# Kernel optimization log

Measured on AMD Instinct MI355X. Metric: run time of the kernel, lower is better.

The kernel has to match this reference:

```python
import jax, jax.numpy as jnp
import numpy as np
from jax import lax

NUM_CLASSES = 5
CONF_THRESH = 0.6
NMS_THRESH = 0.2
NUM_TOPK = 64          # min(topk=1000, 64) as in post_process
STRIDES = (8, 16, 32)
FMP = ((160, 160), (80, 80), (40, 40))  # 1280x1280 input
BATCH = 128


def setup_inputs() -> dict:
    key = jax.random.key(0)
    ks = jax.random.split(key, 9)
    d = {}
    i = 0
    for name, (h, w) in zip(("8", "16", "32"), FMP):
        hw = h * w
        d["obj" + name] = jax.random.normal(ks[i], (BATCH, hw, 1), jnp.float32); i += 1
        d["cls" + name] = jax.random.normal(ks[i], (BATCH, hw, NUM_CLASSES), jnp.float32); i += 1
        d["reg" + name] = jax.random.normal(ks[i], (BATCH, hw, 4), jnp.float32); i += 1
    return d


def make_anchors(h, w, stride):
    ay, ax = jnp.meshgrid(jnp.arange(h), jnp.arange(w), indexing="ij")
    xy = jnp.stack([ax, ay], axis=-1).astype(jnp.float32).reshape(-1, 2)
    return (xy + 0.5) * stride  # [HW, 2]


def decode_boxes(reg, anchors, stride):
    # ctr = reg[:, :2]*stride + anchor;  wh = exp(reg[:, 2:])*stride
    ctr = reg[:, :2] * stride + anchors
    wh = jnp.exp(reg[:, 2:]) * stride
    return jnp.concatenate([ctr - 0.5 * wh, ctr + 0.5 * wh], axis=-1)  # x1y1x2y2


def iou_matrix(b):
    # Faithful to YOLO.nms: areas un-clamped, intersection w/h clamped at 1e-10
    x1, y1, x2, y2 = b[:, 0], b[:, 1], b[:, 2], b[:, 3]
    areas = (x2 - x1) * (y2 - y1)
    xx1 = jnp.maximum(x1[:, None], x1[None, :])
    yy1 = jnp.maximum(y1[:, None], y1[None, :])
    xx2 = jnp.minimum(x2[:, None], x2[None, :])
    yy2 = jnp.minimum(y2[:, None], y2[None, :])
    w = jnp.maximum(1e-10, xx2 - xx1)
    h = jnp.maximum(1e-10, yy2 - yy1)
    inter = w * h
    return inter / (areas[:, None] + areas[None, :] - inter)


def nms_keep(iou, valid):
    # Greedy NMS on score-sorted candidates: fixed-length sequential suppression.
    n = iou.shape[0]
    idx = jnp.arange(n)
    def body(i, keep):
        sup = keep[i] & (iou[i] > NMS_THRESH) & (idx > i)
        return keep & jnp.logical_not(sup)
    return lax.fori_loop(0, n, body, valid)


def _single_image(obj8, cls8, reg8, obj16, cls16, reg16, obj32, cls32, reg32):
    levels = ((obj8, cls8, reg8), (obj16, cls16, reg16), (obj32, cls32, reg32))
    sc, lb, bx, vd = [], [], [], []
    for lvl, (obj, cls, reg) in enumerate(levels):
        h, w = FMP[lvl]
        s = STRIDES[lvl]
        anchors = make_anchors(h, w, s)
        boxes = decode_boxes(reg, anchors, s)                      # [HW, 4]
        scores = jnp.sqrt(jax.nn.sigmoid(obj) * jax.nn.sigmoid(cls)).reshape(-1)  # [HW*C]
        top_s, top_i = lax.top_k(scores, NUM_TOPK)
        a_idx = top_i // NUM_CLASSES
        labels = top_i % NUM_CLASSES
        sc.append(top_s)
        lb.append(labels)
        bx.append(boxes[a_idx])
        vd.append(top_s > CONF_THRESH)
    scores = jnp.concatenate(sc)          # [192]
    labels = jnp.concatenate(lb)
    boxes = jnp.concatenate(bx)           # [192, 4]
    valid = jnp.concatenate(vd)
    # Global score order (within each class this matches the per-class argsort)
    order = jnp.argsort(-scores)
    scores, labels, boxes, valid = scores[order], labels[order], boxes[order], valid[order]
    # Class-offset trick: boxes of different classes have IoU ~ 0 -> exactly per-class NMS
    off = labels.astype(jnp.float32) * (2.0 * jnp.max(jnp.abs(boxes)) + 1.0)
    keep = nms_keep(iou_matrix(boxes + off[:, None]), valid)
    scores = jnp.where(keep, scores, 0.0)
    boxes = jnp.where(keep[:, None], boxes, 0.0)
    labels = jnp.where(keep, labels, -1)
    return boxes, scores, labels


def reference(obj8, cls8, reg8, obj16, cls16, reg16, obj32, cls32, reg32):
    # Batched (vmapped) version of inference_single_image's decode+postprocess.
    # Returns fixed-size masked outputs: boxes [B,192,4], scores [B,192], labels [B,192].
    return jax.vmap(_single_image)(obj8, cls8, reg8, obj16, cls16, reg16, obj32, cls32, reg32)
```

## Files before the change

kernel.cpp:

```cpp
#include <hip/hip_runtime.h>


#define NUM_CLASSES 5
#define CONF_THRESH 0.6f
#define NMS_THRESH  0.2f
#define TOPK   64
#define BATCH  128
#define TOTK   192
#define NCH    21
#define CHUNK  1600
#define SCAP   2048
#define SOFT   448
#define NTHR   320
#define WCAP   1600

typedef unsigned long long u64;
typedef unsigned int u32;

__device__ void bitonic_desc(u64* k, int m) {
  for (int kk = 2; kk <= m; kk <<= 1) {
    for (int j = kk >> 1; j > 0; j >>= 1) {
      __syncthreads();
      for (int i = threadIdx.x; i < m; i += blockDim.x) {
        int ixj = i ^ j;
        if (ixj > i) {
          u64 a = k[i], b = k[ixj];
          bool sw = ((i & kk) == 0) ? (a < b) : (a > b);
          if (sw) { k[i] = b; k[ixj] = a; }
        }
      }
    }
  }
  __syncthreads();
}

__device__ inline u32 wave_sort64_desc_u32(u32 v, int lane) {
  #pragma unroll
  for (int k = 2; k <= 64; k <<= 1) {
    #pragma unroll
    for (int j = k >> 1; j > 0; j >>= 1) {
      u32 o = __shfl_xor(v, j, 64);
      bool keepMax = (((lane & k) == 0) != ((lane & j) != 0));
      v = keepMax ? (v > o ? v : o) : (v < o ? v : o);
    }
  }
  return v;
}

__device__ __forceinline__ u64 u64max(u64 a, u64 b) { return a > b ? a : b; }
__device__ __forceinline__ u64 u64min(u64 a, u64 b) { return a < b ? a : b; }

__device__ __forceinline__ u64 bmerge64_desc(u64 v, int lane) {
  #pragma unroll
  for (int j = 32; j > 0; j >>= 1) {
    u64 o = __shfl_xor(v, j, 64);
    v = ((lane & j) == 0) ? u64max(v, o) : u64min(v, o);
  }
  return v;
}

__device__ __forceinline__ u64 merge_top64(u64 a, u64 brev, int lane) {
  return bmerge64_desc(u64max(a, brev), lane);
}

__device__ __forceinline__ u64 merge4_top64(u64 a, u64 brev, u64 c, u64 drev, int lane) {
  u64 ab = merge_top64(a, brev, lane);
  u64 cd = merge_top64(c, drev, lane);
  u64 cdr = __shfl(cd, 63 - lane, 64);
  return merge_top64(ab, cdr, lane);
}

__device__ inline u64 score_key(float so, float cv, int idx) {
  float sc = 1.0f / (1.0f + expf(-cv));
  float s  = sqrtf(__fmul_rn(so, sc));
  return ((u64)__float_as_uint(s) << 32) | (u32)(~(u32)idx);
}

__device__ inline float sigmoidf(float x) { return 1.0f / (1.0f + expf(-x)); }

__global__ __launch_bounds__(NTHR) void scan_kernel(
    const float* __restrict__ obj8,  const float* __restrict__ cls8,
    const float* __restrict__ obj16, const float* __restrict__ cls16,
    const float* __restrict__ obj32, const float* __restrict__ cls32,
    u64* __restrict__ ws_part) {
  __shared__ u64 keys[SCAP];
  __shared__ u32 wl[WCAP];
  __shared__ int cnt;
  __shared__ int wcnt;
  __shared__ u32 sthr[5];

  const int bx  = blockIdx.x;
  const int img = bx / NCH;
  const int c   = bx - img * NCH;
  const int t   = threadIdx.x;
  const int lane = t & 63, wv = t >> 6;

  const float *obj, *cls;
  int hw, off;
  if (c < 16)      { obj = obj8;  cls = cls8;  hw = 25600; off = c * CHUNK; }
  else if (c < 20) { obj = obj16; cls = cls16; hw = 6400;  off = (c - 16) * CHUNK; }
  else             { obj = obj32; cls = cls32; hw = 1600;  off = 0; }
  obj += (size_t)img * hw + off;
  cls += ((size_t)img * hw + off) * NUM_CLASSES;

  float ff[25];
  {
    #pragma unroll
    for (int a = 0; a < 5; ++a) {
      float o = obj[a * NTHR + t];
      float dob = 1.0f + __expf(-o);
      #pragma unroll
      for (int j = 0; j < 5; ++j) {
        float cvv = cls[(a * NTHR + t) * 5 + j];
        ff[a * 5 + j] = dob * (1.0f + __expf(-cvv));
      }
    }
  }
  float pmin = ff[0];
  #pragma unroll
  for (int i = 1; i < 25; ++i) pmin = fminf(pmin, ff[i]);
  u32 srt = wave_sort64_desc_u32(__float_as_uint(pmin), lane);
  if (lane == 48) sthr[wv] = srt;
  if (t == 0) { cnt = 0; wcnt = 0; }
  __syncthreads();
  u64 thr; float thr_inv;
  {
    float pmax = __uint_as_float(sthr[0]);
    pmax = fmaxf(pmax, __uint_as_float(sthr[1]));
    pmax = fmaxf(pmax, __uint_as_float(sthr[2]));
    pmax = fmaxf(pmax, __uint_as_float(sthr[3]));
    pmax = fmaxf(pmax, __uint_as_float(sthr[4]));
    float ts = sqrtf(__fdiv_rn(1.0f, pmax)) * (1.0f - 1e-4f);
    thr = ((u64)__float_as_uint(ts) << 32) - 1ull;
    thr_inv = __fdiv_rn(1.0f, __fmul_rn(__fmul_rn(ts, ts), 1.0f - 2e-4f));
  }

  int cs = 0;
  #pragma unroll
  for (int a = 0; a < 5; ++a) {
    #pragma unroll
    for (int j = 0; j < 5; ++j) {
      if (ff[a * 5 + j] <= thr_inv) {
        int p = atomicAdd(&wcnt, 1);
        wl[p] = (u32)(((a * NTHR + t) << 3) | j);
      }
    }
    __syncthreads();
    int wc = wcnt;
    for (int i = t; i < wc; i += NTHR) {
      u32 cd = wl[i];
      int al = (int)(cd >> 3);
      int jj = (int)(cd & 7u);
      float o   = obj[al];
      float cvv = cls[al * 5 + jj];
      u64 key = score_key(sigmoidf(o), cvv, (off + al) * NUM_CLASSES + jj);
      if (key > thr) { int p = atomicAdd(&cnt, 1); if (p < SCAP) keys[p] = key; }
    }
    __syncthreads();
    if (t == 0) wcnt = 0;
    cs = cnt;
    __syncthreads();
    if (cs > SOFT) {
      int m = 64; while (m < cs) m <<= 1;
      for (int i = cs + t; i < m; i += NTHR) keys[i] = 0ull;
      bitonic_desc(keys, m);
      if (t == 0) cnt = TOPK;
      u64 nt = keys[TOPK - 1];
      __syncthreads();
      thr = nt; cs = TOPK;
      float tsc = __uint_as_float((u32)(nt >> 32));
      thr_inv = __fdiv_rn(1.0f, __fmul_rn(__fmul_rn(tsc, tsc), 1.0f - 2e-4f));
    }
  }

  {
    int m = 64; while (m < cs) m <<= 1;
    for (int i = cs + t; i < m; i += NTHR) keys[i] = 0ull;
    bitonic_desc(keys, m);
  }
  if (t < TOPK) ws_part[(size_t)bx * TOPK + t] = keys[t];
}

__global__ __launch_bounds__(256) void merge_nms_kernel(
    const u64* __restrict__ ws_part,
    const float* __restrict__ reg8, const float* __restrict__ reg16, const float* __restrict__ reg32,
    float* __restrict__ out) {
  __shared__ u64   lds_runs[256];
  __shared__ u64   lvlkeys[TOTK];
  __shared__ u64   skeys[TOTK];
  __shared__ int   slb[TOTK];
  __shared__ float sbx[TOTK * 4];
  __shared__ float sX1[TOTK], sY1[TOTK], sX2[TOTK], sY2[TOTK], sA[TOTK];
  __shared__ u64   rows[TOTK * 3];
  __shared__ u64   svalid[3];
  __shared__ u64   skeep[3];
  __shared__ float lmarr[3];

  const int img  = blockIdx.x;
  const int t    = threadIdx.x;
  const int lane = t & 63, wv = t >> 6;

  const u64* pbase = ws_part + (size_t)img * NCH * TOPK;

  {
    const u64* q = pbase + (size_t)(4 * wv) * TOPK;
    u64 a    = q[lane];
    u64 brev = q[64 + 63 - lane];
    u64 c    = q[128 + lane];
    u64 drev = q[192 + 63 - lane];
    lds_runs[wv * 64 + lane] = merge4_top64(a, brev, c, drev, lane);
    if (wv == 3) lvlkeys[128 + lane] = pbase[20 * TOPK + lane];
  }
  __syncthreads();

  if (wv == 0) {
    u64 a    = lds_runs[lane];
    u64 brev = lds_runs[64 + 63 - lane];
    u64 c    = lds_runs[128 + lane];
    u64 drev = lds_runs[192 + 63 - lane];
    lvlkeys[lane] = merge4_top64(a, brev, c, drev, lane);
  } else if (wv == 1) {
    const u64* q = pbase + (size_t)16 * TOPK;
    u64 a    = q[lane];
    u64 brev = q[64 + 63 - lane];
    u64 c    = q[128 + lane];
    u64 drev = q[192 + 63 - lane];
    lvlkeys[64 + lane] = merge4_top64(a, brev, c, drev, lane);
  }
  __syncthreads();

  if (wv == 0) {
    const u64 HIMASK = 0xFFFFFFFF00000000ull;
    u64 s0 = (lvlkeys[lane] & HIMASK) | (u32)(~(u32)lane);
    int i1 = 64 + 63 - lane;
    u64 s1r = (lvlkeys[i1] & HIMASK) | (u32)(~(u32)i1);
    int i2 = 128 + 63 - lane;
    u64 s2r = (lvlkeys[i2] & HIMASK) | (u32)(~(u32)i2);
    u64 hi_ = bmerge64_desc(u64max(s0, s1r), lane);
    u64 lo_ = bmerge64_desc(u64min(s0, s1r), lane);
    u64 R1   = u64max(lo_, s2r);
    u64 out0 = bmerge64_desc(u64max(hi_, R1), lane);
    u64 out1 = bmerge64_desc(u64min(hi_, R1), lane);
    u64 out2 = bmerge64_desc(u64min(lo_, s2r), lane);
    skeys[lane]       = out0;
    skeys[64 + lane]  = out1;
    skeys[128 + lane] = out2;
  } else {
    int idx = t - 64;
    const float* reg; int w; int hw; float stride;
    if (wv == 1)      { reg = reg8;  w = 160; hw = 25600; stride = 8.0f;  }
    else if (wv == 2) { reg = reg16; w = 80;  hw = 6400;  stride = 16.0f; }
    else              { reg = reg32; w = 40;  hw = 1600;  stride = 32.0f; }
    reg += (size_t)img * hw * 4;
    u64 key = lvlkeys[idx];
    u32 raw = ~((u32)key);
    int a = (int)(raw / NUM_CLASSES);
    int c = (int)(raw - (u32)a * NUM_CLASSES);
    int ix = a % w, iy = a / w;
    float ax = __fmul_rn((float)ix + 0.5f, stride);
    float ay = __fmul_rn((float)iy + 0.5f, stride);
    float r0 = reg[a*4+0], r1 = reg[a*4+1], r2 = reg[a*4+2], r3 = reg[a*4+3];
    float cx = __fadd_rn(__fmul_rn(r0, stride), ax);
    float cy = __fadd_rn(__fmul_rn(r1, stride), ay);
    float wd = __fmul_rn(expf(r2), stride);
    float ht = __fmul_rn(expf(r3), stride);
    float x1 = __fsub_rn(cx, __fmul_rn(0.5f, wd));
    float y1 = __fsub_rn(cy, __fmul_rn(0.5f, ht));
    float x2 = __fadd_rn(cx, __fmul_rn(0.5f, wd));
    float y2 = __fadd_rn(cy, __fmul_rn(0.5f, ht));
    slb[idx] = c;
    sbx[idx*4+0] = x1; sbx[idx*4+1] = y1;
    sbx[idx*4+2] = x2; sbx[idx*4+3] = y2;
  }
  __syncthreads();

  float sc_r = 0.0f, b0 = 0.0f, b1 = 0.0f, b2 = 0.0f, b3 = 0.0f;
  int p = 0, lb_r = 0;
  if (t < TOTK) {
    u64 key = skeys[t];
    p = (int)(~((u32)key)) & 255;
    sc_r = __uint_as_float((u32)(key >> 32));
    lb_r = slb[p];
    b0 = sbx[p*4+0]; b1 = sbx[p*4+1]; b2 = sbx[p*4+2]; b3 = sbx[p*4+3];
    float lm = fmaxf(fmaxf(fabsf(b0), fabsf(b1)), fmaxf(fabsf(b2), fabsf(b3)));
    #pragma unroll
    for (int d = 32; d > 0; d >>= 1) lm = fmaxf(lm, __shfl_xor(lm, d, 64));
    if (lane == 0) lmarr[wv] = lm;
  }
  __syncthreads();

  const float lmAll = fmaxf(fmaxf(lmarr[0], lmarr[1]), lmarr[2]);
  const float offscale = __fadd_rn(__fmul_rn(2.0f, lmAll), 1.0f);

  float X1 = 0.0f, Y1 = 0.0f, X2 = 0.0f, Y2 = 0.0f, A = 0.0f;
  if (t < TOTK) {
    float off = __fmul_rn((float)lb_r, offscale);
    X1 = __fadd_rn(b0, off); Y1 = __fadd_rn(b1, off);
    X2 = __fadd_rn(b2, off); Y2 = __fadd_rn(b3, off);
    A  = __fmul_rn(__fsub_rn(X2, X1), __fsub_rn(Y2, Y1));
    sX1[t] = X1; sY1[t] = Y1; sX2[t] = X2; sY2[t] = Y2; sA[t] = A;
    u64 bal = __ballot(sc_r > CONF_THRESH);
    if (lane == 0) svalid[wv] = bal;
  }
  __syncthreads();

  if (t < TOTK) {
    u64 r0m = 0, r1m = 0, r2m = 0;
    for (int j = t + 1; j < TOTK; ++j) {
      float xx1 = fmaxf(X1, sX1[j]);
      float yy1 = fmaxf(Y1, sY1[j]);
      float xx2 = fminf(X2, sX2[j]);
      float yy2 = fminf(Y2, sY2[j]);
      float wv2 = fmaxf(1e-10f, __fsub_rn(xx2, xx1));
      float hv = fmaxf(1e-10f, __fsub_rn(yy2, yy1));
      float inter = __fmul_rn(wv2, hv);
      float den = __fsub_rn(__fadd_rn(A, sA[j]), inter);
      float iou = __fdiv_rn(inter, den);
      if (iou > NMS_THRESH) {
        u64 b = 1ull << (j & 63);
        int wd = j >> 6;
        r0m |= (wd == 0) ? b : 0ull;
        r1m |= (wd == 1) ? b : 0ull;
        r2m |= (wd == 2) ? b : 0ull;
      }
    }
    rows[t*3+0] = r0m; rows[t*3+1] = r1m; rows[t*3+2] = r2m;
  }
  __syncthreads();

  if (t < 64) {
    u64 k0 = svalid[0], k1 = svalid[1], k2 = svalid[2];
    #pragma unroll 4
    for (int i = 0; i < 64; ++i) {
      u64 m0 = rows[i*3+0], m1 = rows[i*3+1], m2 = rows[i*3+2];
      u64 sel = 0ull - ((k0 >> i) & 1ull);
      k0 &= ~(m0 & sel); k1 &= ~(m1 & sel); k2 &= ~(m2 & sel);
    }
    #pragma unroll 4
    for (int i = 0; i < 64; ++i) {
      int r = 64 + i;
      u64 m0 = rows[r*3+0], m1 = rows[r*3+1], m2 = rows[r*3+2];
      u64 sel = 0ull - ((k1 >> i) & 1ull);
      k0 &= ~(m0 & sel); k1 &= ~(m1 & sel); k2 &= ~(m2 & sel);
    }
    #pragma unroll 4
    for (int i = 0; i < 64; ++i) {
      int r = 128 + i;
      u64 m0 = rows[r*3+0], m1 = rows[r*3+1], m2 = rows[r*3+2];
      u64 sel = 0ull - ((k2 >> i) & 1ull);
      k0 &= ~(m0 & sel); k1 &= ~(m1 & sel); k2 &= ~(m2 & sel);
    }
    if (t == 0) { skeep[0] = k0; skeep[1] = k1; skeep[2] = k2; }
  }
  __syncthreads();

  if (t < TOTK) {
    float* out_boxes  = out;
    float* out_scores = out + (size_t)BATCH * TOTK * 4;
    float* out_labels = out + (size_t)BATCH * TOTK * 5;
    bool kp = (skeep[t >> 6] >> (t & 63)) & 1ull;
    int gi = img * TOTK + t;
    out_boxes[gi*4+0] = kp ? sbx[p*4+0] : 0.0f;
    out_boxes[gi*4+1] = kp ? sbx[p*4+1] : 0.0f;
    out_boxes[gi*4+2] = kp ? sbx[p*4+2] : 0.0f;
    out_boxes[gi*4+3] = kp ? sbx[p*4+3] : 0.0f;
    out_scores[gi] = kp ? sc_r : 0.0f;
    out_labels[gi] = kp ? (float)lb_r : -1.0f;
  }
}

extern "C" void kernel_launch(void* const* d_in, const int* in_sizes, int n_in,
                              void* d_out, int out_size, void* d_ws, size_t ws_size,
                              hipStream_t stream) {
  const float* obj8  = (const float*)d_in[0];
  const float* cls8  = (const float*)d_in[1];
  const float* reg8  = (const float*)d_in[2];
  const float* obj16 = (const float*)d_in[3];
  const float* cls16 = (const float*)d_in[4];
  const float* reg16 = (const float*)d_in[5];
  const float* obj32 = (const float*)d_in[6];
  const float* cls32 = (const float*)d_in[7];
  const float* reg32 = (const float*)d_in[8];

  u64* ws_part = (u64*)d_ws;

  scan_kernel<<<dim3(BATCH * NCH), dim3(NTHR), 0, stream>>>(
      obj8, cls8, obj16, cls16, obj32, cls32, ws_part);
  merge_nms_kernel<<<dim3(BATCH), dim3(256), 0, stream>>>(
      ws_part, reg8, reg16, reg32, (float*)d_out);
}
```

Before: 240.1 us.

## Vectorize chunk loads, collect candidates in one pass, sort top-64 with wave merges

The per-chunk top-k kernel now loads class and objectness data with float4 reads, so each thread owns four contiguous anchors plus one tail anchor. Candidate filtering becomes a single pass with one barrier, replacing five rounds each with its own barriers and soft bitonic pruning. When the candidate count is small, a full block bitonic sort is replaced by per-wave 64-element register sorts and a tree of top-64 merges. The trade-offs: the candidate buffer can grow larger without intermediate pruning, and there is a fallback path for worklist overflow.

```diff
diff --git a/kernel.cpp b/kernel.cpp
--- a/kernel.cpp
+++ b/kernel.cpp
@@ -10,7 +10,6 @@
 #define NCH    21
 #define CHUNK  1600
 #define SCAP   2048
-#define SOFT   448
 #define NTHR   320
 #define WCAP   1600
 
@@ -47,6 +46,19 @@
   return v;
 }
 
+__device__ inline u64 wave_sort64_desc(u64 v, int lane) {
+  #pragma unroll
+  for (int k = 2; k <= 64; k <<= 1) {
+    #pragma unroll
+    for (int j = k >> 1; j > 0; j >>= 1) {
+      u64 o = __shfl_xor(v, j, 64);
+      bool keepMax = (((lane & k) == 0) != ((lane & j) != 0));
+      v = keepMax ? (v > o ? v : o) : (v < o ? v : o);
+    }
+  }
+  return v;
+}
+
 __device__ __forceinline__ u64 u64max(u64 a, u64 b) { return a > b ? a : b; }
 __device__ __forceinline__ u64 u64min(u64 a, u64 b) { return a < b ? a : b; }
 
@@ -105,17 +117,28 @@
 
   float ff[25];
   {
-    #pragma unroll
-    for (int a = 0; a < 5; ++a) {
-      float o = obj[a * NTHR + t];
-      float dob = 1.0f + __expf(-o);
+    const float4* c4 = (const float4*)cls + (size_t)t * 5;
+    float4 q0 = c4[0], q1 = c4[1], q2 = c4[2], q3 = c4[3], q4 = c4[4];
+    float4 ov = ((const float4*)obj)[t];
+    float cv[20] = { q0.x,q0.y,q0.z,q0.w, q1.x,q1.y,q1.z,q1.w,
+                     q2.x,q2.y,q2.z,q2.w, q3.x,q3.y,q3.z,q3.w,
+                     q4.x,q4.y,q4.z,q4.w };
+    float dob[4] = { 1.0f + __expf(-ov.x), 1.0f + __expf(-ov.y),
+                     1.0f + __expf(-ov.z), 1.0f + __expf(-ov.w) };
+    #pragma unroll
+    for (int a = 0; a < 4; ++a)
       #pragma unroll
-      for (int j = 0; j < 5; ++j) {
-        float cvv = cls[(a * NTHR + t) * 5 + j];
-        ff[a * 5 + j] = dob * (1.0f + __expf(-cvv));
-      }
-    }
-  }
+      for (int j = 0; j < 5; ++j)
+        ff[a * 5 + j] = dob[a] * (1.0f + __expf(-cv[a * 5 + j]));
+    float ot = obj[1280 + t];
+    float dot_ = 1.0f + __expf(-ot);
+    #pragma unroll
+    for (int j = 0; j < 5; ++j) {
+      float cvt = cls[(1280 + t) * 5 + j];
+      ff[20 + j] = dot_ * (1.0f + __expf(-cvt));
+    }
+  }
+
   float pmin = ff[0];
   #pragma unroll
   for (int i = 1; i < 25; ++i) pmin = fminf(pmin, ff[i]);
@@ -135,18 +158,24 @@
     thr_inv = __fdiv_rn(1.0f, __fmul_rn(__fmul_rn(ts, ts), 1.0f - 2e-4f));
   }
 
-  int cs = 0;
-  #pragma unroll
-  for (int a = 0; a < 5; ++a) {
-    #pragma unroll
-    for (int j = 0; j < 5; ++j) {
+  #pragma unroll
+  for (int a = 0; a < 4; ++a)
+    #pragma unroll
+    for (int j = 0; j < 5; ++j)
       if (ff[a * 5 + j] <= thr_inv) {
         int p = atomicAdd(&wcnt, 1);
-        wl[p] = (u32)(((a * NTHR + t) << 3) | j);
+        if (p < WCAP) wl[p] = (u32)(((4 * t + a) << 3) | j);
       }
-    }
-    __syncthreads();
-    int wc = wcnt;
+  #pragma unroll
+  for (int j = 0; j < 5; ++j)
+    if (ff[20 + j] <= thr_inv) {
+      int p = atomicAdd(&wcnt, 1);
+      if (p < WCAP) wl[p] = (u32)(((1280 + t) << 3) | j);
+    }
+  __syncthreads();
+  const int wc = wcnt;
+
+  if (wc <= WCAP) {
     for (int i = t; i < wc; i += NTHR) {
       u32 cd = wl[i];
       int al = (int)(cd >> 3);
@@ -156,27 +185,54 @@
       u64 key = score_key(sigmoidf(o), cvv, (off + al) * NUM_CLASSES + jj);
       if (key > thr) { int p = atomicAdd(&cnt, 1); if (p < SCAP) keys[p] = key; }
     }
-    __syncthreads();
-    if (t == 0) wcnt = 0;
-    cs = cnt;
-    __syncthreads();
-    if (cs > SOFT) {
-      int m = 64; while (m < cs) m <<= 1;
-      for (int i = cs + t; i < m; i += NTHR) keys[i] = 0ull;
-      bitonic_desc(keys, m);
-      if (t == 0) cnt = TOPK;
-      u64 nt = keys[TOPK - 1];
-      __syncthreads();
-      thr = nt; cs = TOPK;
-      float tsc = __uint_as_float((u32)(nt >> 32));
-      thr_inv = __fdiv_rn(1.0f, __fmul_rn(__fmul_rn(tsc, tsc), 1.0f - 2e-4f));
-    }
-  }
-
-  {
+  } else {
+    #pragma unroll
+    for (int a = 0; a < 4; ++a)
+      #pragma unroll
+      for (int j = 0; j < 5; ++j)
+        if (ff[a * 5 + j] <= thr_inv) {
+          int al = 4 * t + a;
+          u64 key = score_key(sigmoidf(obj[al]), cls[al * 5 + j],
+                              (off + al) * NUM_CLASSES + j);
+          if (key > thr) { int p = atomicAdd(&cnt, 1); if (p < SCAP) keys[p] = key; }
+        }
+    #pragma unroll
+    for (int j = 0; j < 5; ++j)
+      if (ff[20 + j] <= thr_inv) {
+        int al = 1280 + t;
+        u64 key = score_key(sigmoidf(obj[al]), cls[al * 5 + j],
+                            (off + al) * NUM_CLASSES + j);
+        if (key > thr) { int p = atomicAdd(&cnt, 1); if (p < SCAP) keys[p] = key; }
+      }
+  }
+  __syncthreads();
+  int cs = cnt; if (cs > SCAP) cs = SCAP;
+  __syncthreads();
+
+  if (cs > 512) {
     int m = 64; while (m < cs) m <<= 1;
     for (int i = cs + t; i < m; i += NTHR) keys[i] = 0ull;
     bitonic_desc(keys, m);
+  } else {
+    int npow = 1; while (npow * 64 < cs) npow <<= 1;
+    for (int i = cs + t; i < npow * 64; i += NTHR) keys[i] = 0ull;
+    __syncthreads();
+    for (int r = wv; r < npow; r += 5) {
+      u64 v = wave_sort64_desc(keys[r * 64 + lane], lane);
+      keys[r * 64 + lane] = v;
+    }
+    __syncthreads();
+    for (int half = npow >> 1; half >= 1; half >>= 1) {
+      u64 res = 0ull;
+      if (wv < half) {
+        u64 a    = keys[(2 * wv) * 64 + lane];
+        u64 brev = keys[(2 * wv + 1) * 64 + 63 - lane];
+        res = merge_top64(a, brev, lane);
+      }
+      __syncthreads();
+      if (wv < half) keys[wv * 64 + lane] = res;
+      __syncthreads();
+    }
   }
   if (t < TOPK) ws_part[(size_t)bx * TOPK + t] = keys[t];
 }
```

Measured after the change: 217.6 us. -9.4%, faster.
